# Kernel optimization log

Hardware: AMD Instinct MI355X
Metric: run time of the kernel (lower is better)

Reference implementation:

```python
import math
import jax, jax.numpy as jnp
import numpy as np

H = 12
D = 64  # head dim

def _heads(x):
    # [b, n, h*d] -> [b, h, n, d]
    b, n, _ = x.shape
    return x.reshape(b, n, H, D).transpose(0, 2, 1, 3)

def setup_inputs() -> dict:
    key = jax.random.key(0)
    ks = jax.random.split(key, 9)
    hs = 768
    s = 1.0 / math.sqrt(hs)
    return {
        "query_states": jax.random.normal(ks[0], (8, 1024, hs), jnp.float32),
        "key_states": jax.random.normal(ks[1], (8, 1024, hs), jnp.float32),
        "Wd": jax.random.normal(ks[2], (hs, hs), jnp.float32) * s,
        "Wq": jax.random.normal(ks[3], (hs, hs), jnp.float32) * s,
        "bq": jax.random.normal(ks[4], (hs,), jnp.float32) * 0.01,
        "Wk": jax.random.normal(ks[5], (hs, hs), jnp.float32) * s,
        "bk": jax.random.normal(ks[6], (hs,), jnp.float32) * 0.01,
        "Wv": jax.random.normal(ks[7], (hs, hs), jnp.float32) * s,
        "bv": jax.random.normal(ks[8], (hs,), jnp.float32) * 0.01,
    }

def reference(query_states, key_states, Wd, Wq, bq, Wk, bk, Wv, bv):
    # projections (torch Linear: x @ W.T + b)
    qd = _heads(query_states @ Wd.T)          # [b,h,n,d]
    kd = _heads(key_states @ Wd.T)
    q = _heads(query_states @ Wq.T + bq)
    k = _heads(key_states @ Wk.T + bk)
    v = _heads(key_states @ Wv.T + bv)
    # -0.5 * cdist(qd, kd)^2 = -0.5*(|qd|^2 + |kd|^2) + qd@kd^T
    qd_sq = jnp.sum(qd * qd, axis=-1)          # [b,h,n]
    kd_sq = jnp.sum(kd * kd, axis=-1)          # [b,h,m]
    quad = (qd @ jnp.swapaxes(kd, -1, -2)
            - 0.5 * qd_sq[..., :, None]
            - 0.5 * kd_sq[..., None, :])       # [b,h,n,m]
    lin = q @ jnp.swapaxes(k, -1, -2)          # [b,h,n,m]
    scores = (quad + lin) / math.sqrt(D)
    probs = jax.nn.softmax(scores, axis=-1)
    ctx = probs @ v                            # [b,h,n,d]
    b, _, n, _ = ctx.shape
    return ctx.transpose(0, 2, 1, 3).reshape(b, n, H * D)
```

## Files before the change

kernel.cpp:

```cpp
#include <hip/hip_runtime.h>
#include <stdint.h>

typedef __attribute__((ext_vector_type(8))) short short8;
typedef __attribute__((ext_vector_type(4))) short short4v;
typedef __attribute__((ext_vector_type(4))) float f32x4;
typedef __attribute__((ext_vector_type(16))) float f32x16;
typedef __attribute__((ext_vector_type(4))) int int4v;

static __device__ __forceinline__ unsigned short f2b(float f) {
  unsigned int u = __builtin_bit_cast(unsigned int, f);
  u += 0x7fffu + ((u >> 16) & 1u);
  return (unsigned short)(u >> 16);
}
static __device__ __forceinline__ float b2f(unsigned short b) {
  unsigned int u = ((unsigned int)b) << 16;
  return __builtin_bit_cast(float, u);
}

#define GLD16(gp, lp)                                                          \
  __builtin_amdgcn_global_load_lds(                                            \
      (const __attribute__((address_space(1))) void*)(gp),                     \
      (__attribute__((address_space(3))) void*)(lp), 16, 0, 0)

#define MFMA16 __builtin_amdgcn_mfma_f32_16x16x32_bf16
#define MFMA32 __builtin_amdgcn_mfma_f32_32x32x16_bf16

#define CVTPK(dst, lo, hi)                                                     \
  asm("v_cvt_pk_bf16_f32 %0, %1, %2" : "=v"(dst) : "v"(lo), "v"(hi))
#define PLSWAP(x, y)                                                           \
  asm volatile("v_permlane32_swap_b32 %0, %1" : "+v"(x), "+v"(y))

#define QSC 0.18033688011112113f
#define C2 0.09016844005556057f

__global__ void cvtx_kernel(const float* __restrict__ q,
                            const float* __restrict__ k,
                            unsigned short* __restrict__ Xq,
                            unsigned short* __restrict__ Xk) {
  const int bx = blockIdx.x;
  const bool lo = bx < 6144;
  const float* src = lo ? q : k;
  unsigned short* dst = lo ? Xq : Xk;
  const int i = (lo ? bx : bx - 6144) * 256 + threadIdx.x;
  float4 v = reinterpret_cast<const float4*>(src)[i];
  short4v o;
  o.x = (short)f2b(v.x);
  o.y = (short)f2b(v.y);
  o.z = (short)f2b(v.z);
  o.w = (short)f2b(v.w);
  reinterpret_cast<short4v*>(dst)[i] = o;
}

__global__ void cvtw_kernel(const float* __restrict__ Wd,
                            const float* __restrict__ Wq,
                            const float* __restrict__ Wk,
                            const float* __restrict__ Wv,
                            unsigned short* __restrict__ Wcq,
                            unsigned short* __restrict__ Wck) {
  const int bx = blockIdx.x;
  const int seg = bx / 576;
  const int i = (bx - seg * 576) * 256 + threadIdx.x;
  const float* src;
  unsigned short* dst;
  switch (seg) {
    case 0: src = Wd; dst = Wcq; break;
    case 1: src = Wq; dst = Wcq + 589824; break;
    case 2: src = Wd; dst = Wck; break;
    case 3: src = Wk; dst = Wck + 589824; break;
    default: src = Wv; dst = Wck + 1179648; break;
  }
  float4 v = reinterpret_cast<const float4*>(src)[i];
  short4v o;
  o.x = (short)f2b(v.x);
  o.y = (short)f2b(v.y);
  o.z = (short)f2b(v.z);
  o.w = (short)f2b(v.w);
  reinterpret_cast<short4v*>(dst)[i] = o;
}

__global__ __launch_bounds__(256) void proj_kernel(
    const unsigned short* __restrict__ Xq, const unsigned short* __restrict__ Xk,
    const unsigned short* __restrict__ Wcq, const unsigned short* __restrict__ Wck,
    const float* __restrict__ bq, const float* __restrict__ bk,
    const float* __restrict__ bv, unsigned short* __restrict__ Qc,
    unsigned short* __restrict__ Kc, unsigned short* __restrict__ Vt) {
  __shared__ __align__(16) short lds[3][2][128 * 32];
  const int by = blockIdx.y;
  const bool mode0 = (by < 12);
  const unsigned short* X = mode0 ? Xq : Xk;
  const unsigned short* W = mode0 ? Wcq : Wck;
  const int col0 = (mode0 ? by : by - 12) * 128;
  const int row0 = blockIdx.x * 128;
  const int lane = threadIdx.x & 63;
  const int w = threadIdx.x >> 6;
  const int wr = w >> 1, wc = w & 1;
  const int l15 = lane & 15, l4 = lane >> 4;

  f32x4 acc[4][4];
#pragma unroll
  for (int i = 0; i < 4; ++i)
#pragma unroll
    for (int j = 0; j < 4; ++j) acc[i][j] = (f32x4){0.f, 0.f, 0.f, 0.f};

  auto stage = [&](int bufi, int k0) {
#pragma unroll
    for (int iss = 0; iss < 2; ++iss) {
      const int c = iss * 256 + w * 64 + lane;
      const int r = c >> 2;
      const int sl = (c & 3) ^ (r & 3);
      const unsigned short* gp = X + (size_t)(row0 + r) * 768 + k0 + sl * 8;
      GLD16(gp, (char*)&lds[bufi][0][0] + (iss * 256 + w * 64) * 16);
    }
#pragma unroll
    for (int iss = 0; iss < 2; ++iss) {
      const int c = iss * 256 + w * 64 + lane;
      const int r = c >> 2;
      const int sl = (c & 3) ^ (r & 3);
      const unsigned short* gp = W + (size_t)(col0 + r) * 768 + k0 + sl * 8;
      GLD16(gp, (char*)&lds[bufi][1][0] + (iss * 256 + w * 64) * 16);
    }
  };

  stage(0, 0);
  stage(1, 32);

#pragma unroll 3
  for (int kt = 0; kt < 24; ++kt) {
    if (kt < 23) {
      asm volatile("s_waitcnt vmcnt(4)" ::: "memory");
    } else {
      asm volatile("s_waitcnt vmcnt(0)" ::: "memory");
    }
    __syncthreads();
    if (kt < 22) stage((kt + 2) % 3, (kt + 2) * 32);

    const char* Ab = (const char*)&lds[kt % 3][0][0];
    const char* Bb = (const char*)&lds[kt % 3][1][0];
    short8 a[4], b[4];
#pragma unroll
    for (int mt = 0; mt < 4; ++mt) {
      const int r = wr * 64 + mt * 16 + l15;
      a[mt] = *reinterpret_cast<const short8*>(Ab + r * 64 +
                                               ((l4 ^ (r & 3)) << 4));
    }
#pragma unroll
    for (int nt = 0; nt < 4; ++nt) {
      const int r = wc * 64 + nt * 16 + l15;
      b[nt] = *reinterpret_cast<const short8*>(Bb + r * 64 +
                                               ((l4 ^ (r & 3)) << 4));
    }
#pragma unroll
    for (int mt = 0; mt < 4; ++mt)
#pragma unroll
      for (int nt = 0; nt < 4; ++nt)
        acc[mt][nt] = MFMA16(a[mt], b[nt], acc[mt][nt], 0, 0, 0);
  }

  const int mat = mode0 ? (col0 >= 768 ? 1 : 0) : (col0 / 768);
  const int cbase = col0 - mat * 768 + wc * 64;
  const float* barr = mode0 ? bq : (mat == 2 ? bv : bk);
  if (!mode0 && mat == 2) {
#pragma unroll
    for (int nt = 0; nt < 4; ++nt) {
      const int cc = cbase + nt * 16 + l15;
      const int hh = cc >> 6, dd = cc & 63;
      const float bias = barr[cc];
#pragma unroll
      for (int mt = 0; mt < 4; ++mt) {
        const int row = row0 + wr * 64 + mt * 16 + l4 * 4;
        const int bb = row >> 10, nn = row & 1023;
        short4v pv;
#pragma unroll
        for (int i = 0; i < 4; ++i)
          pv[i] = (short)f2b(acc[mt][nt][i] + bias);
        *reinterpret_cast<short4v*>(
            Vt + ((size_t)(bb * 12 + hh) * 64 + dd) * 1024 + nn) = pv;
      }
    }
  } else {
    const float scale = mode0 ? QSC : 1.0f;
    unsigned short* outC = mode0 ? Qc : Kc;
#pragma unroll
    for (int nt = 0; nt < 4; ++nt) {
      const int cc = cbase + nt * 16 + l15;
      const int hh = cc >> 6, dd = cc & 63;
      const float bias = (mat >= 1) ? barr[cc] : 0.f;
#pragma unroll
      for (int mt = 0; mt < 4; ++mt) {
#pragma unroll
        for (int i = 0; i < 4; ++i) {
          const int row = row0 + wr * 64 + mt * 16 + l4 * 4 + i;
          const int bb = row >> 10, nn = row & 1023;
          outC[((size_t)(bb * 12 + hh) * 1024 + nn) * 128 + mat * 64 + dd] =
              f2b((acc[mt][nt][i] + bias) * scale);
        }
      }
    }
  }
}

__global__ __launch_bounds__(256) void wv_kernel(
    const unsigned short* __restrict__ Kc, unsigned short* __restrict__ wq,
    const unsigned short* __restrict__ Vt, unsigned short* __restrict__ Vs) {
  __shared__ float wf[1024];
  const int bh = blockIdx.x;
  const int t = threadIdx.x;
  const int part = t & 3;
  const unsigned short* Kb = Kc + (size_t)bh * 1024 * 128;
#pragma unroll
  for (int it = 0; it < 16; ++it) {
    const int key = it * 64 + (t >> 2);
    const short8* p =
        reinterpret_cast<const short8*>(Kb + (size_t)key * 128 + part * 16);
    float s = 0.f;
    short8 x0 = p[0], x1 = p[1];
#pragma unroll
    for (int j = 0; j < 8; ++j) {
      const float f0 = b2f((unsigned short)x0[j]);
      const float f1 = b2f((unsigned short)x1[j]);
      s += f0 * f0 + f1 * f1;
    }
    s += __shfl_xor(s, 1);
    s += __shfl_xor(s, 2);
    if (part == 0) {
      const unsigned short wb = f2b(__builtin_amdgcn_exp2f(-s * C2));
      wf[key] = b2f(wb);
      wq[(size_t)bh * 1024 + key] = wb;
    }
  }
  __syncthreads();
  const unsigned short* Vb = Vt + (size_t)bh * 64 * 1024;
  unsigned short* Ob = Vs + (size_t)bh * 64 * 1024;
#pragma unroll
  for (int i = 0; i < 32; ++i) {
    const int e0 = (i * 256 + t) * 8;
    const int k0 = e0 & 1023;
    short8 v = *reinterpret_cast<const short8*>(Vb + e0);
#pragma unroll
    for (int j = 0; j < 8; ++j)
      v[j] = (short)f2b(b2f((unsigned short)v[j]) * wf[k0 + j]);
    *reinterpret_cast<short8*>(Ob + e0) = v;
  }
}

__global__ __launch_bounds__(256, 3) void attn_kernel(
    const unsigned short* __restrict__ Qc, const unsigned short* __restrict__ Kc,
    const unsigned short* __restrict__ Vs, const unsigned short* __restrict__ wq,
    float* __restrict__ out) {
  __shared__ __align__(16) short kbuf[2][64 * 128];
  __shared__ __align__(16) short vbuf[2][64 * 64];
  __shared__ __align__(16) short wbuf[1024];

  const int bh = blockIdx.x % 96;
  const int qb = blockIdx.x / 96;
  const int b = bh / 12, h = bh - b * 12;
  const int lane = threadIdx.x & 63;
  const int w = threadIdx.x >> 6;
  const int l31 = lane & 31, l5 = lane >> 5;

  const unsigned short* Kg = Kc + (size_t)bh * 1024 * 128;
  const unsigned short* Vg = Vs + (size_t)bh * 64 * 1024;

  auto stageK = [&](int bufi, int kb) {
#pragma unroll
    for (int i = 0; i < 4; ++i) {
      const int slot = i * 256 + threadIdx.x;
      const int row = slot >> 4;
      const int d0 = ((slot & 15) ^ (row & 15)) * 8;
      const unsigned short* gp = Kg + (size_t)(kb * 64 + row) * 128 + d0;
      GLD16(gp, (char*)(&kbuf[bufi][0]) + (i * 256 + w * 64) * 16);
    }
  };
  auto stageV = [&](int bufi, int kb) {
#pragma unroll
    for (int i = 0; i < 2; ++i) {
      const int slot = i * 256 + threadIdx.x;
      const int row = slot >> 3;
      const int k0 = ((slot & 7) ^ (row & 7)) * 8;
      const unsigned short* gp = Vg + (size_t)row * 1024 + kb * 64 + k0;
      GLD16(gp, (char*)(&vbuf[bufi][0]) + (i * 256 + w * 64) * 16);
    }
  };

  stageK(0, 0);
  stageV(0, 0);
  if (w < 2) {
    const unsigned short* gp = wq + (size_t)bh * 1024 + (w * 64 + lane) * 8;
    GLD16(gp, (char*)(&wbuf[0]) + w * 1024);
  }

  const unsigned short* Qb =
      Qc + ((size_t)bh * 1024 + qb * 128 + w * 32 + l31) * 128 + l5 * 8;
  short8 qf[8];
#pragma unroll
  for (int s = 0; s < 8; ++s)
    qf[s] = *reinterpret_cast<const short8*>(Qb + s * 16);

  f32x16 o0, o1, la;
#pragma unroll
  for (int r = 0; r < 16; ++r) {
    o0[r] = 0.f;
    o1[r] = 0.f;
    la[r] = 0.f;
  }
  float m = -1e30f;

  const int S4 = (lane & 15) << 4;
  const int S3 = (lane & 7) << 4;
  const int ko = l5 * 16;

  asm volatile("s_waitcnt vmcnt(0)" ::: "memory");
  __syncthreads();

  int buf = 0;
  for (int kb = 0; kb < 16; ++kb) {
    if (kb < 15) {
      stageK(buf ^ 1, kb + 1);
      stageV(buf ^ 1, kb + 1);
    }

    const char* kB = (const char*)(&kbuf[buf][0]) + l31 * 256;
    f32x16 s0, s1;
#pragma unroll
    for (int r = 0; r < 16; ++r) {
      s0[r] = 0.f;
      s1[r] = 0.f;
    }
#pragma unroll
    for (int s = 0; s < 8; ++s) {
      const int off = (s * 32 + ko) ^ S4;
      short8 a0 = *reinterpret_cast<const short8*>(kB + off);
      short8 a1 = *reinterpret_cast<const short8*>(kB + 8192 + off);
      s0 = MFMA32(a0, qf[s], s0, 0, 0, 0);
      s1 = MFMA32(a1, qf[s], s1, 0, 0, 0);
    }

    float mx = s0[0];
#pragma unroll
    for (int r = 1; r < 16; ++r) mx = fmaxf(mx, s0[r]);
#pragma unroll
    for (int r = 0; r < 16; ++r) mx = fmaxf(mx, s1[r]);
    mx = fmaxf(mx, __shfl_xor(mx, 32));

    if (!__all(mx <= m + 11.0f)) {
      const float mn = fmaxf(m, mx);
      const float c = __builtin_amdgcn_exp2f(m - mn);
      m = mn;
      float cr[16];
#pragma unroll
      for (int r = 0; r < 16; ++r)
        cr[r] = __shfl(c, (r & 3) + 8 * (r >> 2) + 4 * l5);
#pragma unroll
      for (int r = 0; r < 16; ++r) {
        la[r] *= cr[r];
        o0[r] *= cr[r];
        o1[r] *= cr[r];
      }
    }

#pragma unroll
    for (int r = 0; r < 16; ++r) {
      s0[r] = __builtin_amdgcn_exp2f(s0[r] - m);
      s1[r] = __builtin_amdgcn_exp2f(s1[r] - m);
    }
    unsigned int u[16];
#pragma unroll
    for (int j = 0; j < 8; ++j) {
      CVTPK(u[j], s0[2 * j], s0[2 * j + 1]);
      CVTPK(u[8 + j], s1[2 * j], s1[2 * j + 1]);
    }
    PLSWAP(u[0], u[2]);
    PLSWAP(u[1], u[3]);
    PLSWAP(u[4], u[6]);
    PLSWAP(u[5], u[7]);
    PLSWAP(u[8], u[10]);
    PLSWAP(u[9], u[11]);
    PLSWAP(u[12], u[14]);
    PLSWAP(u[13], u[15]);
    short8 pa[4];
    {
      int4v t0 = {(int)u[0], (int)u[1], (int)u[2], (int)u[3]};
      int4v t1 = {(int)u[4], (int)u[5], (int)u[6], (int)u[7]};
      int4v t2 = {(int)u[8], (int)u[9], (int)u[10], (int)u[11]};
      int4v t3 = {(int)u[12], (int)u[13], (int)u[14], (int)u[15]};
      pa[0] = __builtin_bit_cast(short8, t0);
      pa[1] = __builtin_bit_cast(short8, t1);
      pa[2] = __builtin_bit_cast(short8, t2);
      pa[3] = __builtin_bit_cast(short8, t3);
    }

    const char* vB = (const char*)(&vbuf[buf][0]) + l31 * 128;
    const char* wB = (const char*)(&wbuf[0]) + kb * 128 + ko;
#pragma unroll
    for (int kk = 0; kk < 4; ++kk) {
      const int off = (kk * 32 + ko) ^ S3;
      short8 v0 = *reinterpret_cast<const short8*>(vB + off);
      short8 v1 = *reinterpret_cast<const short8*>(vB + 4096 + off);
      short8 wf = *reinterpret_cast<const short8*>(wB + kk * 32);
      o0 = MFMA32(pa[kk], v0, o0, 0, 0, 0);
      o1 = MFMA32(pa[kk], v1, o1, 0, 0, 0);
      la = MFMA32(pa[kk], wf, la, 0, 0, 0);
    }

    asm volatile("s_waitcnt vmcnt(0)" ::: "memory");
    __syncthreads();
    buf ^= 1;
  }

  const int qbase = b * 1024 + qb * 128 + w * 32;
#pragma unroll
  for (int r = 0; r < 16; ++r) {
    const float iv = __builtin_amdgcn_rcpf(la[r]);
    const int q = qbase + (r & 3) + 8 * (r >> 2) + 4 * l5;
    float* op = out + (size_t)q * 768 + h * 64 + l31;
    op[0] = o0[r] * iv;
    op[32] = o1[r] * iv;
  }
}

extern "C" void kernel_launch(void* const* d_in, const int* in_sizes, int n_in,
                              void* d_out, int out_size, void* d_ws,
                              size_t ws_size, hipStream_t stream) {
  const float* query = (const float*)d_in[0];
  const float* key = (const float*)d_in[1];
  const float* Wd = (const float*)d_in[2];
  const float* Wq = (const float*)d_in[3];
  const float* bq = (const float*)d_in[4];
  const float* Wk = (const float*)d_in[5];
  const float* bk = (const float*)d_in[6];
  const float* Wv = (const float*)d_in[7];
  const float* bv = (const float*)d_in[8];
  float* out = (float*)d_out;

  char* p = (char*)d_ws;
  auto alloc = [&](size_t n) {
    char* r = p;
    p += (n + 255) & ~(size_t)255;
    return r;
  };
  unsigned short* Xq = (unsigned short*)alloc(8192ULL * 768 * 2);
  unsigned short* Xk = (unsigned short*)alloc(8192ULL * 768 * 2);
  unsigned short* Wcq = (unsigned short*)alloc(1536ULL * 768 * 2);
  unsigned short* Wck = (unsigned short*)alloc(2304ULL * 768 * 2);
  unsigned short* Qc = (unsigned short*)alloc(96ULL * 1024 * 128 * 2);
  unsigned short* Kc = (unsigned short*)alloc(96ULL * 1024 * 128 * 2);
  unsigned short* Vt = (unsigned short*)alloc(96ULL * 64 * 1024 * 2);
  unsigned short* wqv = (unsigned short*)alloc(96ULL * 1024 * 2);
  unsigned short* Vs = Xk;

  cvtx_kernel<<<12288, 256, 0, stream>>>(query, key, Xq, Xk);
  cvtw_kernel<<<2880, 256, 0, stream>>>(Wd, Wq, Wk, Wv, Wcq, Wck);

  proj_kernel<<<dim3(64, 30), 256, 0, stream>>>(Xq, Xk, Wcq, Wck, bq, bk, bv,
                                                Qc, Kc, Vt);

  wv_kernel<<<96, 256, 0, stream>>>(Kc, wqv, Vt, Vs);

  attn_kernel<<<768, 256, 0, stream>>>(Qc, Kc, Vs, wqv, out);
}
```

Before: 164.0 us.

## Enlarge projection GEMM tile to 256x256 with 8 waves per block

The projection GEMM tile grows from 128x128 to 256x256. Blocks now run 512 threads with 8 waves, each wave computing 128x64, and the grid shrinks from 64x30 to 32x15. This raises arithmetic intensity and reuse of each LDS-staged tile, cutting global and LDS traffic per FLOP. The LDS swizzle is changed to a lane-based pattern, and the barrier is replaced with a raw s_barrier plus an explicit lgkmcnt wait. The costs are more LDS (96KB per block), higher register pressure from 32 accumulators, and only 480 blocks, which may leave the 256 CUs unevenly loaded.

```diff
diff --git a/kernel.cpp b/kernel.cpp
--- a/kernel.cpp
+++ b/kernel.cpp
@@ -78,46 +78,49 @@
   reinterpret_cast<short4v*>(dst)[i] = o;
 }
 
-__global__ __launch_bounds__(256) void proj_kernel(
+__global__ __launch_bounds__(512, 2) void proj_kernel(
     const unsigned short* __restrict__ Xq, const unsigned short* __restrict__ Xk,
     const unsigned short* __restrict__ Wcq, const unsigned short* __restrict__ Wck,
     const float* __restrict__ bq, const float* __restrict__ bk,
     const float* __restrict__ bv, unsigned short* __restrict__ Qc,
     unsigned short* __restrict__ Kc, unsigned short* __restrict__ Vt) {
-  __shared__ __align__(16) short lds[3][2][128 * 32];
+  __shared__ __align__(16) short lds[3][2][256 * 32];
   const int by = blockIdx.y;
-  const bool mode0 = (by < 12);
+  const bool mode0 = (by < 6);
   const unsigned short* X = mode0 ? Xq : Xk;
   const unsigned short* W = mode0 ? Wcq : Wck;
-  const int col0 = (mode0 ? by : by - 12) * 128;
-  const int row0 = blockIdx.x * 128;
-  const int lane = threadIdx.x & 63;
-  const int w = threadIdx.x >> 6;
-  const int wr = w >> 1, wc = w & 1;
+  const int col0 = (mode0 ? by : by - 6) * 256;
+  const int row0 = blockIdx.x * 256;
+  const int tid = threadIdx.x;
+  const int lane = tid & 63;
+  const int wid = tid >> 6;
+  const int wm = wid >> 2;
+  const int wn = wid & 3;
   const int l15 = lane & 15, l4 = lane >> 4;
-
-  f32x4 acc[4][4];
-#pragma unroll
-  for (int i = 0; i < 4; ++i)
+  const int RSWZ = (l4 ^ ((l15 >> 1) & 3)) << 4;
+
+  f32x4 acc[8][4];
+#pragma unroll
+  for (int i = 0; i < 8; ++i)
 #pragma unroll
     for (int j = 0; j < 4; ++j) acc[i][j] = (f32x4){0.f, 0.f, 0.f, 0.f};
 
   auto stage = [&](int bufi, int k0) {
 #pragma unroll
     for (int iss = 0; iss < 2; ++iss) {
-      const int c = iss * 256 + w * 64 + lane;
+      const int c = iss * 512 + tid;
       const int r = c >> 2;
-      const int sl = (c & 3) ^ (r & 3);
+      const int sl = (c & 3) ^ ((c >> 3) & 3);
       const unsigned short* gp = X + (size_t)(row0 + r) * 768 + k0 + sl * 8;
-      GLD16(gp, (char*)&lds[bufi][0][0] + (iss * 256 + w * 64) * 16);
+      GLD16(gp, (char*)&lds[bufi][0][0] + (size_t)c * 16);
     }
 #pragma unroll
     for (int iss = 0; iss < 2; ++iss) {
-      const int c = iss * 256 + w * 64 + lane;
+      const int c = iss * 512 + tid;
       const int r = c >> 2;
-      const int sl = (c & 3) ^ (r & 3);
+      const int sl = (c & 3) ^ ((c >> 3) & 3);
       const unsigned short* gp = W + (size_t)(col0 + r) * 768 + k0 + sl * 8;
-      GLD16(gp, (char*)&lds[bufi][1][0] + (iss * 256 + w * 64) * 16);
+      GLD16(gp, (char*)&lds[bufi][1][0] + (size_t)c * 16);
     }
   };
 
@@ -127,37 +130,36 @@
 #pragma unroll 3
   for (int kt = 0; kt < 24; ++kt) {
     if (kt < 23) {
-      asm volatile("s_waitcnt vmcnt(4)" ::: "memory");
+      asm volatile("s_waitcnt vmcnt(4) lgkmcnt(0)" ::: "memory");
     } else {
-      asm volatile("s_waitcnt vmcnt(0)" ::: "memory");
-    }
-    __syncthreads();
+      asm volatile("s_waitcnt vmcnt(0) lgkmcnt(0)" ::: "memory");
+    }
+    __builtin_amdgcn_s_barrier();
+    asm volatile("" ::: "memory");
     if (kt < 22) stage((kt + 2) % 3, (kt + 2) * 32);
 
     const char* Ab = (const char*)&lds[kt % 3][0][0];
     const char* Bb = (const char*)&lds[kt % 3][1][0];
-    short8 a[4], b[4];
-#pragma unroll
-    for (int mt = 0; mt < 4; ++mt) {
-      const int r = wr * 64 + mt * 16 + l15;
-      a[mt] = *reinterpret_cast<const short8*>(Ab + r * 64 +
-                                               ((l4 ^ (r & 3)) << 4));
+    short8 a[8], b[4];
+#pragma unroll
+    for (int mt = 0; mt < 8; ++mt) {
+      const int r = wm * 128 + mt * 16 + l15;
+      a[mt] = *reinterpret_cast<const short8*>(Ab + r * 64 + RSWZ);
     }
 #pragma unroll
     for (int nt = 0; nt < 4; ++nt) {
-      const int r = wc * 64 + nt * 16 + l15;
-      b[nt] = *reinterpret_cast<const short8*>(Bb + r * 64 +
-                                               ((l4 ^ (r & 3)) << 4));
-    }
-#pragma unroll
-    for (int mt = 0; mt < 4; ++mt)
+      const int r = wn * 64 + nt * 16 + l15;
+      b[nt] = *reinterpret_cast<const short8*>(Bb + r * 64 + RSWZ);
+    }
+#pragma unroll
+    for (int mt = 0; mt < 8; ++mt)
 #pragma unroll
       for (int nt = 0; nt < 4; ++nt)
         acc[mt][nt] = MFMA16(a[mt], b[nt], acc[mt][nt], 0, 0, 0);
   }
 
-  const int mat = mode0 ? (col0 >= 768 ? 1 : 0) : (col0 / 768);
-  const int cbase = col0 - mat * 768 + wc * 64;
+  const int mat = mode0 ? (col0 >= 768 ? 1 : 0) : ((by - 6) / 3);
+  const int cbase = col0 - mat * 768 + wn * 64;
   const float* barr = mode0 ? bq : (mat == 2 ? bv : bk);
   if (!mode0 && mat == 2) {
 #pragma unroll
@@ -166,8 +168,8 @@
       const int hh = cc >> 6, dd = cc & 63;
       const float bias = barr[cc];
 #pragma unroll
-      for (int mt = 0; mt < 4; ++mt) {
-        const int row = row0 + wr * 64 + mt * 16 + l4 * 4;
+      for (int mt = 0; mt < 8; ++mt) {
+        const int row = row0 + wm * 128 + mt * 16 + l4 * 4;
         const int bb = row >> 10, nn = row & 1023;
         short4v pv;
 #pragma unroll
@@ -186,10 +188,10 @@
       const int hh = cc >> 6, dd = cc & 63;
       const float bias = (mat >= 1) ? barr[cc] : 0.f;
 #pragma unroll
-      for (int mt = 0; mt < 4; ++mt) {
+      for (int mt = 0; mt < 8; ++mt) {
 #pragma unroll
         for (int i = 0; i < 4; ++i) {
-          const int row = row0 + wr * 64 + mt * 16 + l4 * 4 + i;
+          const int row = row0 + wm * 128 + mt * 16 + l4 * 4 + i;
           const int bb = row >> 10, nn = row & 1023;
           outC[((size_t)(bb * 12 + hh) * 1024 + nn) * 128 + mat * 64 + dd] =
               f2b((acc[mt][nt][i] + bias) * scale);
@@ -451,7 +453,7 @@
   cvtx_kernel<<<12288, 256, 0, stream>>>(query, key, Xq, Xk);
   cvtw_kernel<<<2880, 256, 0, stream>>>(Wd, Wq, Wk, Wv, Wcq, Wck);
 
-  proj_kernel<<<dim3(64, 30), 256, 0, stream>>>(Xq, Xk, Wcq, Wck, bq, bk, bv,
+  proj_kernel<<<dim3(32, 15), 512, 0, stream>>>(Xq, Xk, Wcq, Wck, bq, bk, bv,
                                                 Qc, Kc, Vt);
 
   wv_kernel<<<96, 256, 0, stream>>>(Kc, wqv, Vt, Vs);
```

Result: faster. 155.0 us (-5.5%).
